# Optimization experiments

Measured on AMD Instinct MI355X. Metric: run time of the kernel, lower is better.

## Reference

```python
import jax, jax.numpy as jnp
import numpy as np

B, C, IMG, P, D, H, L, FF, NC = 32, 3, 224, 16, 768, 12, 12, 3072, 14
G = IMG // P            # 14 patches per side
S = G * G + 1           # 197 tokens incl cls
DH = D // H             # 64 head dim


def layer_norm(x, w, b, eps=1e-5):
    m = jnp.mean(x, axis=-1, keepdims=True)
    v = jnp.mean((x - m) ** 2, axis=-1, keepdims=True)
    return (x - m) / jnp.sqrt(v + eps) * w + b


def setup_inputs() -> dict:
    key = jax.random.key(0)
    ks = iter(jax.random.split(key, 32))
    n = lambda s, scale=0.02: jax.random.normal(next(ks), s, dtype=jnp.float32) * scale
    inp = {
        'x': jax.random.normal(next(ks), (B, C, IMG, IMG), dtype=jnp.float32),
        'patch_w': n((D, C, P, P)),
        'patch_b': jnp.zeros((D,), jnp.float32),
        'cls_token': n((1, 1, D)),
        'pos_emb': n((1, S, D)),
        'ln1_w': jnp.ones((L, D), jnp.float32),
        'ln1_b': jnp.zeros((L, D), jnp.float32),
        'wq': n((L, D, D)), 'bq': jnp.zeros((L, D), jnp.float32),
        'wk': n((L, D, D)), 'bk': jnp.zeros((L, D), jnp.float32),
        'wv': n((L, D, D)), 'bv': jnp.zeros((L, D), jnp.float32),
        'wo': n((L, D, D)), 'bo': jnp.zeros((L, D), jnp.float32),
        'ln2_w': jnp.ones((L, D), jnp.float32),
        'ln2_b': jnp.zeros((L, D), jnp.float32),
        'fc1_w': n((L, FF, D)), 'fc1_b': jnp.zeros((L, FF), jnp.float32),
        'fc2_w': n((L, D, FF)), 'fc2_b': jnp.zeros((L, D), jnp.float32),
        'clf_w': n((NC, D)), 'clf_b': jnp.zeros((NC,), jnp.float32),
    }
    return inp


def _vit_forward(x, patch_w, patch_b, cls_token, pos_emb,
                 ln1_w, ln1_b, wq, bq, wk, bk, wv, bv, wo, bo,
                 ln2_w, ln2_b, fc1_w, fc1_b, fc2_w, fc2_b, clf_w, clf_b):
    b = x.shape[0]
    # Patch embed: stride==kernel conv == reshape to patches + matmul.
    patches = x.reshape(b, C, G, P, G, P).transpose(0, 2, 4, 1, 3, 5).reshape(b, G * G, C * P * P)
    emb = patches @ patch_w.reshape(D, -1).T + patch_b            # [b, 196, D]
    h = jnp.concatenate([jnp.broadcast_to(cls_token, (b, 1, D)), emb], axis=1) + pos_emb

    def block(h, p):
        l1w, l1b, Wq, Bq, Wk, Bk, Wv, Bv, Wo, Bo, l2w, l2b, F1w, F1b, F2w, F2b = p
        y = layer_norm(h, l1w, l1b)
        q = (y @ Wq.T + Bq).reshape(b, S, H, DH)
        k = (y @ Wk.T + Bk).reshape(b, S, H, DH)
        v = (y @ Wv.T + Bv).reshape(b, S, H, DH)
        scores = jnp.einsum('bqhd,bkhd->bhqk', q, k) / np.sqrt(DH).astype(np.float32)
        a = jax.nn.softmax(scores, axis=-1)
        o = jnp.einsum('bhqk,bkhd->bqhd', a, v).reshape(b, S, D)
        h = h + (o @ Wo.T + Bo)
        y = layer_norm(h, l2w, l2b)
        h = h + jax.nn.gelu(y @ F1w.T + F1b, approximate=False) @ F2w.T + F2b
        return h, None

    params = (ln1_w, ln1_b, wq, bq, wk, bk, wv, bv, wo, bo,
              ln2_w, ln2_b, fc1_w, fc1_b, fc2_w, fc2_b)
    h, _ = jax.lax.scan(block, h, params)
    logits = h[:, 0] @ clf_w.T + clf_b                            # [b, NC]
    return logits


def reference(x, patch_w, patch_b, cls_token, pos_emb,
              ln1_w, ln1_b, wq, bq, wk, bk, wv, bv, wo, bo,
              ln2_w, ln2_b, fc1_w, fc1_b, fc2_w, fc2_b, clf_w, clf_b):
    return _vit_forward(x, patch_w, patch_b, cls_token, pos_emb,
                        ln1_w, ln1_b, wq, bq, wk, bk, wv, bv, wo, bo,
                        ln2_w, ln2_b, fc1_w, fc1_b, fc2_w, fc2_b, clf_w, clf_b)
```

## Files before the change

kernel.cpp:

```cpp
#include <hip/hip_runtime.h>
#include <hip/hip_bf16.h>
#include <cstdint>
#include <cstddef>

typedef __attribute__((ext_vector_type(8))) short  bf16x8;
typedef __attribute__((ext_vector_type(4))) float  f32x4;
typedef __attribute__((ext_vector_type(4))) ushort u16x4;
typedef __attribute__((ext_vector_type(8))) ushort u16x8;

#define MFMA16(a, b, c) __builtin_amdgcn_mfma_f32_16x16x32_bf16((a), (b), (c), 0, 0, 0)

__device__ __forceinline__ ushort f2b(float x) {
    union { float f; uint32_t u; } c; c.f = x;
    uint32_t u = c.u + 0x7fffu + ((c.u >> 16) & 1u);
    return (ushort)(u >> 16);
}

__device__ __forceinline__ void gload_lds16(const ushort* g, ushort* l) {
    __builtin_amdgcn_global_load_lds((const __attribute__((address_space(1))) void*)g,
                                     (__attribute__((address_space(3))) void*)l, 16, 0, 0);
}

template<int BM, int BN, int OUTBF, int RES, int GELU>
__global__ __launch_bounds__(256)
void gemm_bt(const ushort* __restrict__ A, const ushort* __restrict__ W,
             const float* __restrict__ bias, const float* resid,
             void* outp, int M, int N, int K, int gx)
{
    constexpr int NI   = BM / 32;
    constexpr int NJ   = BN / 32;
    constexpr int NCHA = BM / 16;
    constexpr int NCHB = BN / 16;
    constexpr int NCH  = 2 * (NCHA + NCHB);
    constexpr int PER  = NCH / 4;
    __shared__ __align__(16) ushort Als[2][2 * NCHA * 512];
    __shared__ __align__(16) ushort Bls[2][2 * NCHB * 512];

    const int tid  = threadIdx.x;
    const int lane = tid & 63, wid = tid >> 6;

    const int nwg  = gridDim.x;
    const int orig = blockIdx.x;
    const int xcd = orig & 7, local = orig >> 3;
    const int q8 = nwg >> 3, r8 = nwg & 7;
    const int swz = (xcd < r8 ? xcd * (q8 + 1) : r8 * (q8 + 1) + (xcd - r8) * q8) + local;
    const int bx = swz % gx, by = swz / gx;

    const int m0 = by * BM, n0 = bx * BN;
    const int wr = wid >> 1, wc = wid & 1;
    const int ecol = lane & 15, eg = lane >> 4;

    const int dec  = lane ^ ((lane >> 3) & 7);
    const int srow = dec >> 2;
    const int scol = (dec & 3) * 8;

    const int sfrag = ecol * 4 + eg;
    const int swslot = sfrag ^ ((sfrag >> 3) & 7);

    f32x4 acc[NI][NJ] = {};

    auto stage = [&](int p, int k0) {
#pragma unroll
        for (int c = 0; c < PER; ++c) {
            const int q = wid * PER + c;
            if (q < 2 * NCHA) {
                const int rg = q >> 1, kh = q & 1;
                const int row = rg * 16 + srow;
                int ga = m0 + row; if (ga > M - 1) ga = M - 1;
                gload_lds16(A + (size_t)ga * K + k0 + kh * 32 + scol, &Als[p][q * 512]);
            } else {
                const int qq = q - 2 * NCHA;
                const int rg = qq >> 1, kh = qq & 1;
                gload_lds16(W + (size_t)(n0 + rg * 16 + srow) * K + k0 + kh * 32 + scol,
                            &Bls[p][qq * 512]);
            }
        }
    };

    const int NT = K >> 6;
    stage(0, 0);
    __syncthreads();

    int cur = 0;
    for (int t = 0; t < NT; ++t) {
        if (t + 1 < NT) stage(cur ^ 1, (t + 1) << 6);
#pragma unroll
        for (int kk = 0; kk < 2; ++kk) {
            bf16x8 af[NI], bfr[NJ];
#pragma unroll
            for (int i = 0; i < NI; ++i)
                af[i] = *(const bf16x8*)&Als[cur][(((wr * NI + i) << 1) + kk) * 512 + swslot * 8];
#pragma unroll
            for (int j = 0; j < NJ; ++j)
                bfr[j] = *(const bf16x8*)&Bls[cur][(((wc * NJ + j) << 1) + kk) * 512 + swslot * 8];
#pragma unroll
            for (int i = 0; i < NI; ++i)
#pragma unroll
                for (int j = 0; j < NJ; ++j)
                    acc[i][j] = MFMA16(af[i], bfr[j], acc[i][j]);
        }
        if (t + 1 < NT) __syncthreads();
        cur ^= 1;
    }

#pragma unroll
    for (int i = 0; i < NI; ++i) {
        const int mb = m0 + wr * (BM / 2) + i * 16 + eg * 4;
#pragma unroll
        for (int j = 0; j < NJ; ++j) {
            const int n = n0 + wc * (BN / 2) + j * 16 + ecol;
            const float bv = bias[n];
#pragma unroll
            for (int r = 0; r < 4; ++r) {
                const int m = mb + r;
                if (m < M) {
                    float v = acc[i][j][r] + bv;
                    if (RES)  v += resid[(size_t)m * N + n];
                    if (GELU) {
                        const float xx = v;
                        const float a = 0.7978845608f * (xx + 0.044715f * xx * xx * xx);
                        const float t2 = 1.0f - 2.0f / (1.0f + __expf(2.0f * a));
                        v = 0.5f * xx * (1.0f + t2);
                    }
                    if (OUTBF) ((ushort*)outp)[(size_t)m * N + n] = f2b(v);
                    else       ((float*)outp)[(size_t)m * N + n]  = v;
                }
            }
        }
    }
}

__global__ __launch_bounds__(256)
void attn_k(const ushort* __restrict__ qkv, ushort* __restrict__ o)
{
    __shared__ __align__(16) ushort Vt[64][224];
    __shared__ __align__(16) ushort Pb[4][16][224];
    const int bh = blockIdx.x;
    const int b = bh / 12, hh = bh % 12;
    const int tid = threadIdx.x, lane = tid & 63, wid = tid >> 6;
    const size_t rs = 2304;
    const ushort* qb = qkv + (size_t)b * 197 * rs + hh * 64;
    const ushort* kb = qb + 768;
    const ushort* vb = qb + 1536;

    for (int i = tid; i < 197 * 64; i += 256) {
        const int s = i >> 6, d = i & 63;
        Vt[d][s] = vb[(size_t)s * rs + d];
    }
    for (int i = tid; i < 64 * 27; i += 256) {
        const int d = i / 27, s = 197 + i % 27;
        Vt[d][s] = 0;
    }
    __syncthreads();

    const int ecol = lane & 15, eg = lane >> 4;
    const bool m12bad = (192 + ecol) > 196;

    for (int qt = wid; qt < 13; qt += 4) {
        int qrow = qt * 16 + ecol; if (qrow > 196) qrow = 196;
        bf16x8 qa0 = *(const bf16x8*)&qb[(size_t)qrow * rs + eg * 8];
        bf16x8 qa1 = *(const bf16x8*)&qb[(size_t)qrow * rs + 32 + eg * 8];

        f32x4 s[13];
#pragma unroll
        for (int kt = 0; kt < 13; ++kt) {
            int krow = kt * 16 + ecol; if (krow > 196) krow = 196;
            bf16x8 kf0 = *(const bf16x8*)&kb[(size_t)krow * rs + eg * 8];
            bf16x8 kf1 = *(const bf16x8*)&kb[(size_t)krow * rs + 32 + eg * 8];
            f32x4 a = {};
            a = MFMA16(qa0, kf0, a);
            a = MFMA16(qa1, kf1, a);
            s[kt] = a;
        }
#pragma unroll
        for (int kt = 0; kt < 13; ++kt)
#pragma unroll
            for (int r = 0; r < 4; ++r) s[kt][r] *= 0.125f;
        if (m12bad) { s[12][0] = -1e30f; s[12][1] = -1e30f; s[12][2] = -1e30f; s[12][3] = -1e30f; }

#pragma unroll
        for (int r = 0; r < 4; ++r) {
            float mx = s[0][r];
#pragma unroll
            for (int kt = 1; kt < 13; ++kt) mx = fmaxf(mx, s[kt][r]);
#pragma unroll
            for (int off = 1; off < 16; off <<= 1) mx = fmaxf(mx, __shfl_xor(mx, off));
            float sm = 0.0f;
#pragma unroll
            for (int kt = 0; kt < 13; ++kt) { float e = __expf(s[kt][r] - mx); s[kt][r] = e; sm += e; }
#pragma unroll
            for (int off = 1; off < 16; off <<= 1) sm += __shfl_xor(sm, off);
            const float inv = 1.0f / sm;
#pragma unroll
            for (int kt = 0; kt < 13; ++kt) s[kt][r] *= inv;
        }

#pragma unroll
        for (int kt = 0; kt < 13; ++kt)
#pragma unroll
            for (int r = 0; r < 4; ++r)
                Pb[wid][eg * 4 + r][kt * 16 + ecol] = f2b(s[kt][r]);
#pragma unroll
        for (int r = 0; r < 4; ++r) Pb[wid][eg * 4 + r][208 + ecol] = 0;
        asm volatile("s_waitcnt lgkmcnt(0)" ::: "memory");
        __builtin_amdgcn_sched_barrier(0);

        f32x4 oacc[4] = {};
#pragma unroll
        for (int ks = 0; ks < 7; ++ks) {
            bf16x8 pa = *(const bf16x8*)&Pb[wid][ecol][ks * 32 + eg * 8];
#pragma unroll
            for (int dt = 0; dt < 4; ++dt) {
                bf16x8 vf = *(const bf16x8*)&Vt[dt * 16 + ecol][ks * 32 + eg * 8];
                oacc[dt] = MFMA16(pa, vf, oacc[dt]);
            }
        }
#pragma unroll
        for (int dt = 0; dt < 4; ++dt)
#pragma unroll
            for (int r = 0; r < 4; ++r) {
                const int q = qt * 16 + eg * 4 + r;
                if (q < 197)
                    o[((size_t)(b * 197 + q)) * 768 + hh * 64 + dt * 16 + ecol] = f2b(oacc[dt][r]);
            }
        asm volatile("s_waitcnt lgkmcnt(0)" ::: "memory");
        __builtin_amdgcn_sched_barrier(0);
    }
}

__global__ __launch_bounds__(256)
void ln_k(const float* __restrict__ x, const float* __restrict__ g,
          const float* __restrict__ bta, ushort* __restrict__ y, int rows)
{
    const int row  = blockIdx.x * 4 + (threadIdx.x >> 6);
    const int lane = threadIdx.x & 63;
    if (row >= rows) return;
    const float* xr = x + (size_t)row * 768;
    f32x4 v[3];
#pragma unroll
    for (int t = 0; t < 3; ++t) v[t] = *(const f32x4*)&xr[(lane + t * 64) * 4];
    float s = 0.0f;
#pragma unroll
    for (int t = 0; t < 3; ++t) s += v[t][0] + v[t][1] + v[t][2] + v[t][3];
#pragma unroll
    for (int off = 1; off < 64; off <<= 1) s += __shfl_xor(s, off);
    const float mean = s * (1.0f / 768.0f);
    float sq = 0.0f;
#pragma unroll
    for (int t = 0; t < 3; ++t)
#pragma unroll
        for (int c = 0; c < 4; ++c) { const float d = v[t][c] - mean; sq += d * d; }
#pragma unroll
    for (int off = 1; off < 64; off <<= 1) sq += __shfl_xor(sq, off);
    const float rstd = rsqrtf(sq * (1.0f / 768.0f) + 1e-5f);
    ushort* yr = y + (size_t)row * 768;
#pragma unroll
    for (int t = 0; t < 3; ++t) {
        const int c0 = (lane + t * 64) * 4;
        f32x4 gw = *(const f32x4*)&g[c0];
        f32x4 bb = *(const f32x4*)&bta[c0];
        u16x4 ov;
#pragma unroll
        for (int c = 0; c < 4; ++c) ov[c] = f2b((v[t][c] - mean) * rstd * gw[c] + bb[c]);
        *(u16x4*)&yr[c0] = ov;
    }
}

__global__ void im2col_k(const float* __restrict__ x, ushort* __restrict__ p)
{
    const int gid = blockIdx.x * 256 + threadIdx.x;
    if (gid >= 6272 * 768) return;
    const int m = gid / 768, idx = gid - m * 768;
    const int b = m / 196, t = m - b * 196;
    const int gy = t / 14, gx = t - gy * 14;
    const int c = idx >> 8, rr = idx & 255;
    const int py = rr >> 4, px = rr & 15;
    const float v = x[(((size_t)(b * 3 + c) * 224) + gy * 16 + py) * 224 + gx * 16 + px];
    p[gid] = f2b(v);
}

__global__ void assemble_k(const float* __restrict__ emb, const float* __restrict__ cls,
                           const float* __restrict__ pos, float* __restrict__ h)
{
    const int gid = blockIdx.x * 256 + threadIdx.x;
    if (gid >= 6304 * 192) return;
    const int r = gid / 192, c4 = gid - r * 192;
    const int b = r / 197, s = r - b * 197;
    f32x4 pe = *(const f32x4*)&pos[(s * 192 + c4) * 4];
    f32x4 sv;
    if (s == 0) sv = *(const f32x4*)&cls[c4 * 4];
    else        sv = *(const f32x4*)&emb[((size_t)(b * 196 + (s - 1)) * 192 + c4) * 4];
    f32x4 ov = pe + sv;
    *(f32x4*)&h[(size_t)gid * 4] = ov;
}

__global__ void cvt_k(const float* __restrict__ src, ushort* __restrict__ dst, int n8)
{
    const int g = blockIdx.x * 256 + threadIdx.x;
    if (g >= n8) return;
    const int e = g * 8;
    f32x4 a = *(const f32x4*)&src[e];
    f32x4 b = *(const f32x4*)&src[e + 4];
    u16x8 ov;
#pragma unroll
    for (int c = 0; c < 4; ++c) { ov[c] = f2b(a[c]); ov[4 + c] = f2b(b[c]); }
    *(u16x8*)&dst[e] = ov;
}

__global__ void conv6_k(const float* __restrict__ s0, const float* __restrict__ s1,
                        const float* __restrict__ s2, const float* __restrict__ s3,
                        const float* __restrict__ s4, const float* __restrict__ s5,
                        ushort* __restrict__ dst)
{
    const int g = blockIdx.x * 256 + threadIdx.x;
    if (g >= 884736) return;
    const int e = g * 8;
    const float* src; int off;
    if      (e < 589824)  { src = s0; off = e; }
    else if (e < 1179648) { src = s1; off = e - 589824; }
    else if (e < 1769472) { src = s2; off = e - 1179648; }
    else if (e < 2359296) { src = s3; off = e - 1769472; }
    else if (e < 4718592) { src = s4; off = e - 2359296; }
    else                  { src = s5; off = e - 4718592; }
    f32x4 a = *(const f32x4*)&src[off];
    f32x4 b = *(const f32x4*)&src[off + 4];
    u16x8 ov;
#pragma unroll
    for (int c = 0; c < 4; ++c) { ov[c] = f2b(a[c]); ov[4 + c] = f2b(b[c]); }
    *(u16x8*)&dst[e] = ov;
}

__global__ void bias3_k(const float* __restrict__ b0, const float* __restrict__ b1,
                        const float* __restrict__ b2, float* __restrict__ dst)
{
    const int i = blockIdx.x * 256 + threadIdx.x;
    if (i >= 2304) return;
    dst[i] = (i < 768) ? b0[i] : (i < 1536 ? b1[i - 768] : b2[i - 1536]);
}

__global__ __launch_bounds__(64)
void clf_k(const float* __restrict__ h, const float* __restrict__ w,
           const float* __restrict__ bias, float* __restrict__ out)
{
    const int b = blockIdx.x, lane = threadIdx.x;
    const float* hr = h + (size_t)b * 197 * 768;
    float hv[12];
#pragma unroll
    for (int j = 0; j < 12; ++j) hv[j] = hr[lane + j * 64];
    for (int n = 0; n < 14; ++n) {
        float sm = 0.0f;
#pragma unroll
        for (int j = 0; j < 12; ++j) sm += hv[j] * w[n * 768 + lane + j * 64];
#pragma unroll
        for (int off = 1; off < 64; off <<= 1) sm += __shfl_xor(sm, off);
        if (lane == 0) out[b * 14 + n] = sm + bias[n];
    }
}

extern "C" void kernel_launch(void* const* d_in, const int* in_sizes, int n_in,
                              void* d_out, int out_size, void* d_ws, size_t ws_size,
                              hipStream_t stream)
{
    const float* x       = (const float*)d_in[0];
    const float* patch_w = (const float*)d_in[1];
    const float* patch_b = (const float*)d_in[2];
    const float* cls_tok = (const float*)d_in[3];
    const float* pos_emb = (const float*)d_in[4];
    const float* ln1_w   = (const float*)d_in[5];
    const float* ln1_b   = (const float*)d_in[6];
    const float* wq      = (const float*)d_in[7];
    const float* bq      = (const float*)d_in[8];
    const float* wk      = (const float*)d_in[9];
    const float* bk      = (const float*)d_in[10];
    const float* wv      = (const float*)d_in[11];
    const float* bv      = (const float*)d_in[12];
    const float* wo      = (const float*)d_in[13];
    const float* bo      = (const float*)d_in[14];
    const float* ln2_w   = (const float*)d_in[15];
    const float* ln2_b   = (const float*)d_in[16];
    const float* fc1w    = (const float*)d_in[17];
    const float* fc1b    = (const float*)d_in[18];
    const float* fc2w    = (const float*)d_in[19];
    const float* fc2b    = (const float*)d_in[20];
    const float* clfw    = (const float*)d_in[21];
    const float* clfb    = (const float*)d_in[22];

    char* ws = (char*)d_ws;
    float*  h    = (float*)(ws + 0);
    ushort* y    = (ushort*)(ws + 19365888);
    ushort* qkv  = (ushort*)(ws + 29048832);
    ushort* o    = (ushort*)(ws + 58097664);
    ushort* ff   = (ushort*)(ws + 67780608);
    ushort* wbuf = (ushort*)(ws + 106512384);
    float*  b3   = (float*)(ws + 120668160);
    ushort* patches = (ushort*)(ws + 67780608);
    float*  emb     = (float*)(ws + 67780608 + 16777216);

    im2col_k<<<18816, 256, 0, stream>>>(x, patches);
    cvt_k<<<288, 256, 0, stream>>>(patch_w, wbuf, 73728);
    gemm_bt<128, 64, 0, 0, 0><<<12 * 49, 256, 0, stream>>>(patches, wbuf, patch_b,
                                                      (const float*)nullptr, (void*)emb, 6272, 768, 768, 12);
    assemble_k<<<4728, 256, 0, stream>>>(emb, cls_tok, pos_emb, h);

    for (int l = 0; l < 12; ++l) {
        conv6_k<<<3456, 256, 0, stream>>>(wq + (size_t)l * 589824, wk + (size_t)l * 589824,
                                          wv + (size_t)l * 589824, wo + (size_t)l * 589824,
                                          fc1w + (size_t)l * 2359296, fc2w + (size_t)l * 2359296, wbuf);
        bias3_k<<<9, 256, 0, stream>>>(bq + l * 768, bk + l * 768, bv + l * 768, b3);
        ln_k<<<1576, 256, 0, stream>>>(h, ln1_w + l * 768, ln1_b + l * 768, y, 6304);
        gemm_bt<128, 64, 1, 0, 0><<<36 * 50, 256, 0, stream>>>(y, wbuf, b3,
                                                           (const float*)nullptr, (void*)qkv, 6304, 2304, 768, 36);
        attn_k<<<384, 256, 0, stream>>>(qkv, o);
        gemm_bt<128, 64, 0, 1, 0><<<12 * 50, 256, 0, stream>>>(o, wbuf + 1769472, bo + l * 768,
                                                          (const float*)h, (void*)h, 6304, 768, 768, 12);
        ln_k<<<1576, 256, 0, stream>>>(h, ln2_w + l * 768, ln2_b + l * 768, y, 6304);
        gemm_bt<128, 64, 1, 0, 1><<<48 * 50, 256, 0, stream>>>(y, wbuf + 2359296, fc1b + (size_t)l * 3072,
                                                           (const float*)nullptr, (void*)ff, 6304, 3072, 768, 48);
        gemm_bt<128, 64, 0, 1, 0><<<12 * 50, 256, 0, stream>>>(ff, wbuf + 4718592, fc2b + l * 768,
                                                          (const float*)h, (void*)h, 6304, 768, 3072, 12);
    }
    clf_k<<<32, 64, 0, stream>>>(h, clfw, clfb, (float*)d_out);
}
```

Measured before the change: 3.295 ms.

## Add 8-wave triple-buffered GEMM with larger tiles for transformer layer matmuls

Adds a new GEMM kernel that runs 512 threads (8 waves) per block. It uses larger output tiles (256x128 and 128x128), a 3-stage LDS ring buffer with explicit vmcnt waits in place of a full syncthreads per k-step, and s_setprio around the MFMA bursts. The four per-layer GEMMs (QKV, out-proj, FC1, FC2) now use it, cutting global reloads of A and B tiles and aiming to overlap loads with compute. In exchange it uses more LDS per block and launches fewer blocks, which may leave some CUs idle and hurt balance, especially on the N=768 GEMMs with only 300 blocks.

```diff
diff --git a/kernel.cpp b/kernel.cpp
--- a/kernel.cpp
+++ b/kernel.cpp
@@ -19,6 +19,119 @@
 __device__ __forceinline__ void gload_lds16(const ushort* g, ushort* l) {
     __builtin_amdgcn_global_load_lds((const __attribute__((address_space(1))) void*)g,
                                      (__attribute__((address_space(3))) void*)l, 16, 0, 0);
+}
+
+__device__ __forceinline__ float gelu_f(float xx) {
+    const float a = 0.7978845608f * (xx + 0.044715f * xx * xx * xx);
+    const float t2 = 1.0f - 2.0f / (1.0f + __expf(2.0f * a));
+    return 0.5f * xx * (1.0f + t2);
+}
+
+template<int BM, int BN, int WM, int WN, int OUTBF, int RES, int GELU>
+__global__ __launch_bounds__(512)
+void gemm8(const ushort* __restrict__ A, const ushort* __restrict__ W,
+           const float* __restrict__ bias, const float* resid,
+           void* outp, int M, int N, int K, int gx)
+{
+    constexpr int NI  = BM / 16 / WM;
+    constexpr int NJ  = BN / 16 / WN;
+    constexpr int NCA = BM / 8;
+    constexpr int NCB = BN / 8;
+    constexpr int PER = (NCA + NCB) / 8;
+    __shared__ __align__(16) ushort Als[3][NCA * 512];
+    __shared__ __align__(16) ushort Bls[3][NCB * 512];
+
+    const int tid  = threadIdx.x;
+    const int lane = tid & 63, wid = tid >> 6;
+
+    const int nwg  = gridDim.x;
+    const int orig = blockIdx.x;
+    const int xcd = orig & 7, local = orig >> 3;
+    const int q8 = nwg >> 3, r8 = nwg & 7;
+    const int swz = (xcd < r8 ? xcd * (q8 + 1) : r8 * (q8 + 1) + (xcd - r8) * q8) + local;
+    const int bx = swz % gx, by = swz / gx;
+
+    const int m0 = by * BM, n0 = bx * BN;
+    const int wr = wid / WN, wc = wid % WN;
+    const int ecol = lane & 15, eg = lane >> 4;
+
+    const int dec  = lane ^ ((lane >> 3) & 7);
+    const int srow = dec >> 2;
+    const int scol = (dec & 3) * 8;
+    const int sfrag = ecol * 4 + eg;
+    const int swslot = sfrag ^ ((sfrag >> 3) & 7);
+
+    f32x4 acc[NI][NJ] = {};
+
+    auto stage = [&](int p, int k0) {
+#pragma unroll
+        for (int c = 0; c < PER; ++c) {
+            const int q = wid * PER + c;
+            if (q < NCA) {
+                const int rg = q >> 1, kh = q & 1;
+                int ga = m0 + rg * 16 + srow; if (ga > M - 1) ga = M - 1;
+                gload_lds16(A + (size_t)ga * K + k0 + kh * 32 + scol, &Als[p][q * 512]);
+            } else {
+                const int qq = q - NCA;
+                const int rg = qq >> 1, kh = qq & 1;
+                gload_lds16(W + (size_t)(n0 + rg * 16 + srow) * K + k0 + kh * 32 + scol,
+                            &Bls[p][qq * 512]);
+            }
+        }
+    };
+
+    const int NT = K >> 6;
+    stage(0, 0);
+
+    for (int t = 0; t < NT; ++t) {
+        if (t + 1 < NT) {
+            stage((t + 1) % 3, (t + 1) << 6);
+            asm volatile("s_waitcnt vmcnt(%0)" :: "n"(PER) : "memory");
+        } else {
+            asm volatile("s_waitcnt vmcnt(0)" ::: "memory");
+        }
+        __builtin_amdgcn_s_barrier();
+        const int cur = t % 3;
+#pragma unroll
+        for (int kk = 0; kk < 2; ++kk) {
+            bf16x8 af[NI], bfr[NJ];
+#pragma unroll
+            for (int i = 0; i < NI; ++i)
+                af[i] = *(const bf16x8*)&Als[cur][(((wr * NI + i) << 1) + kk) * 512 + swslot * 8];
+#pragma unroll
+            for (int j = 0; j < NJ; ++j)
+                bfr[j] = *(const bf16x8*)&Bls[cur][(((wc * NJ + j) << 1) + kk) * 512 + swslot * 8];
+            __builtin_amdgcn_s_setprio(1);
+#pragma unroll
+            for (int i = 0; i < NI; ++i)
+#pragma unroll
+                for (int j = 0; j < NJ; ++j)
+                    acc[i][j] = MFMA16(af[i], bfr[j], acc[i][j]);
+            __builtin_amdgcn_s_setprio(0);
+            __builtin_amdgcn_s_barrier();
+        }
+    }
+
+#pragma unroll
+    for (int i = 0; i < NI; ++i) {
+        const int mb = m0 + wr * (NI * 16) + i * 16 + eg * 4;
+#pragma unroll
+        for (int j = 0; j < NJ; ++j) {
+            const int n = n0 + wc * (NJ * 16) + j * 16 + ecol;
+            const float bv = bias[n];
+#pragma unroll
+            for (int r = 0; r < 4; ++r) {
+                const int m = mb + r;
+                if (m < M) {
+                    float v = acc[i][j][r] + bv;
+                    if (RES)  v += resid[(size_t)m * N + n];
+                    if (GELU) v = gelu_f(v);
+                    if (OUTBF) ((ushort*)outp)[(size_t)m * N + n] = f2b(v);
+                    else       ((float*)outp)[(size_t)m * N + n]  = v;
+                }
+            }
+        }
+    }
 }
 
 template<int BM, int BN, int OUTBF, int RES, int GELU>
@@ -53,7 +166,6 @@
     const int dec  = lane ^ ((lane >> 3) & 7);
     const int srow = dec >> 2;
     const int scol = (dec & 3) * 8;
-
     const int sfrag = ecol * 4 + eg;
     const int swslot = sfrag ^ ((sfrag >> 3) & 7);
 
@@ -65,8 +177,7 @@
             const int q = wid * PER + c;
             if (q < 2 * NCHA) {
                 const int rg = q >> 1, kh = q & 1;
-                const int row = rg * 16 + srow;
-                int ga = m0 + row; if (ga > M - 1) ga = M - 1;
+                int ga = m0 + rg * 16 + srow; if (ga > M - 1) ga = M - 1;
                 gload_lds16(A + (size_t)ga * K + k0 + kh * 32 + scol, &Als[p][q * 512]);
             } else {
                 const int qq = q - 2 * NCHA;
@@ -116,12 +227,7 @@
                 if (m < M) {
                     float v = acc[i][j][r] + bv;
                     if (RES)  v += resid[(size_t)m * N + n];
-                    if (GELU) {
-                        const float xx = v;
-                        const float a = 0.7978845608f * (xx + 0.044715f * xx * xx * xx);
-                        const float t2 = 1.0f - 2.0f / (1.0f + __expf(2.0f * a));
-                        v = 0.5f * xx * (1.0f + t2);
-                    }
+                    if (GELU) v = gelu_f(v);
                     if (OUTBF) ((ushort*)outp)[(size_t)m * N + n] = f2b(v);
                     else       ((float*)outp)[(size_t)m * N + n]  = v;
                 }
@@ -408,16 +514,16 @@
                                           fc1w + (size_t)l * 2359296, fc2w + (size_t)l * 2359296, wbuf);
         bias3_k<<<9, 256, 0, stream>>>(bq + l * 768, bk + l * 768, bv + l * 768, b3);
         ln_k<<<1576, 256, 0, stream>>>(h, ln1_w + l * 768, ln1_b + l * 768, y, 6304);
-        gemm_bt<128, 64, 1, 0, 0><<<36 * 50, 256, 0, stream>>>(y, wbuf, b3,
-                                                           (const float*)nullptr, (void*)qkv, 6304, 2304, 768, 36);
+        gemm8<256, 128, 4, 2, 1, 0, 0><<<18 * 25, 512, 0, stream>>>(y, wbuf, b3,
+                                                           (const float*)nullptr, (void*)qkv, 6304, 2304, 768, 18);
         attn_k<<<384, 256, 0, stream>>>(qkv, o);
-        gemm_bt<128, 64, 0, 1, 0><<<12 * 50, 256, 0, stream>>>(o, wbuf + 1769472, bo + l * 768,
-                                                          (const float*)h, (void*)h, 6304, 768, 768, 12);
+        gemm8<128, 128, 2, 4, 0, 1, 0><<<6 * 50, 512, 0, stream>>>(o, wbuf + 1769472, bo + l * 768,
+                                                          (const float*)h, (void*)h, 6304, 768, 768, 6);
         ln_k<<<1576, 256, 0, stream>>>(h, ln2_w + l * 768, ln2_b + l * 768, y, 6304);
-        gemm_bt<128, 64, 1, 0, 1><<<48 * 50, 256, 0, stream>>>(y, wbuf + 2359296, fc1b + (size_t)l * 3072,
-                                                           (const float*)nullptr, (void*)ff, 6304, 3072, 768, 48);
-        gemm_bt<128, 64, 0, 1, 0><<<12 * 50, 256, 0, stream>>>(ff, wbuf + 4718592, fc2b + l * 768,
-                                                          (const float*)h, (void*)h, 6304, 768, 3072, 12);
+        gemm8<256, 128, 4, 2, 1, 0, 1><<<24 * 25, 512, 0, stream>>>(y, wbuf + 2359296, fc1b + (size_t)l * 3072,
+                                                           (const float*)nullptr, (void*)ff, 6304, 3072, 768, 24);
+        gemm8<128, 128, 2, 4, 0, 1, 0><<<6 * 50, 512, 0, stream>>>(ff, wbuf + 4718592, fc2b + l * 768,
+                                                          (const float*)h, (void*)h, 6304, 768, 3072, 6);
     }
     clf_k<<<32, 64, 0, stream>>>(h, clfw, clfb, (float*)d_out);
 }
```

New measurement: 3.839 ms. +16.5%, slower.
